# Kernel tuning notes

Measured on AMD Instinct MI355X. Metric: run time of the kernel, lower is better.

## Reference

```python
import jax, jax.numpy as jnp
import numpy as np

S, B, D, H, L = 1024, 2, 1024, 16, 4
HD = D // H            # 64
MLP = 4 * D            # 4096
EPS = 1e-5


def _ln(x, w, b):
    m = x.mean(-1, keepdims=True)
    v = ((x - m) ** 2).mean(-1, keepdims=True)
    return (x - m) * jax.lax.rsqrt(v + EPS) * w + b


def _rotate_half(x):
    h = x.shape[-1] // 2
    return jnp.concatenate([-x[..., h:], x[..., :h]], axis=-1)


def _rope(t, cos, sin):
    # t: (B, S, H, HD); cos/sin: (S, HD) broadcast to (1, S, 1, HD)
    return t * cos[None, :, None, :] + _rotate_half(t) * sin[None, :, None, :]


def setup_inputs() -> dict:
    key = jax.random.key(0)
    ks = iter(jax.random.split(key, 64))

    def p(shape, scale=0.02):
        return jax.random.normal(next(ks), shape, jnp.float32) * scale

    return {
        "x": jax.random.normal(next(ks), (S, B, D), jnp.float32),
        "rotary_pos_emb": jax.random.normal(next(ks), (S, HD // 2), jnp.float32),
        # stacked per-layer params (leading dim L) for lax.scan
        "ln1_w": jnp.ones((L, D), jnp.float32), "ln1_b": jnp.zeros((L, D), jnp.float32),
        "in_w": p((L, 3 * D, D)), "in_b": jnp.zeros((L, 3 * D), jnp.float32),
        "out_w": p((L, D, D)), "out_b": jnp.zeros((L, D), jnp.float32),
        "ln2_w": jnp.ones((L, D), jnp.float32), "ln2_b": jnp.zeros((L, D), jnp.float32),
        "fc_w": p((L, MLP, D)), "fc_b": jnp.zeros((L, MLP), jnp.float32),
        "cp_w": p((L, D, MLP)), "cp_b": jnp.zeros((L, D), jnp.float32),
        # attention pooling head (qkv_bias=False in CrossAttention)
        "pn_q_w": jnp.ones((D,), jnp.float32), "pn_q_b": jnp.zeros((D,), jnp.float32),
        "pn_k_w": jnp.ones((D,), jnp.float32), "pn_k_b": jnp.zeros((D,), jnp.float32),
        "pn_v_w": jnp.ones((D,), jnp.float32), "pn_v_b": jnp.zeros((D,), jnp.float32),
        "pq_w": p((D, D)), "pk_w": p((D, D)), "pv_w": p((D, D)),
        "pp_w": p((D, D)), "pp_b": jnp.zeros((D,), jnp.float32),
    }


def reference(x, rotary_pos_emb, ln1_w, ln1_b, in_w, in_b, out_w, out_b,
              ln2_w, ln2_b, fc_w, fc_b, cp_w, cp_b,
              pn_q_w, pn_q_b, pn_k_w, pn_k_b, pn_v_w, pn_v_b,
              pq_w, pk_w, pv_w, pp_w, pp_b):
    # freqs (S, HD/2) -> cos/sin tiled twice along last dim: (S, HD)
    cos = jnp.tile(jnp.cos(rotary_pos_emb), (1, 2))
    sin = jnp.tile(jnp.sin(rotary_pos_emb), (1, 2))
    scale = 1.0 / np.sqrt(HD).astype(np.float32)

    def layer(h, p):
        l1w, l1b, iw, ib, ow, ob, l2w, l2b, fw, fb, cw, cb = p
        a = _ln(h, l1w, l1b)
        qkv = jnp.einsum('sbd,ed->sbe', a, iw) + ib           # (S,B,3D)
        qkv = qkv.reshape(S, B, 3, H, HD)
        q = jnp.transpose(qkv[:, :, 0], (1, 0, 2, 3))          # (B,S,H,HD)
        k = jnp.transpose(qkv[:, :, 1], (1, 0, 2, 3))
        v = jnp.transpose(qkv[:, :, 2], (1, 0, 2, 3))
        q = _rope(q, cos, sin)
        k = _rope(k, cos, sin)
        q, k, v = (t.transpose(0, 2, 1, 3) for t in (q, k, v))  # (B,H,S,HD)
        attn = jax.nn.softmax(jnp.einsum('bhsd,bhtd->bhst', q, k) * scale, axis=-1)
        o = jnp.einsum('bhst,bhtd->bhsd', attn, v)
        o = o.transpose(2, 0, 1, 3).reshape(S, B, D)           # back to (S,B,D)
        h = h + jnp.einsum('sbd,ed->sbe', o, ow) + ob          # residual + out_proj
        m = _ln(h, l2w, l2b)
        m = jax.nn.gelu(jnp.einsum('sbd,ed->sbe', m, fw) + fb, approximate=False)
        h = h + jnp.einsum('sbe,de->sbd', m, cw) + cb          # residual + c_proj
        return h, None

    h, _ = jax.lax.scan(layer, x, (ln1_w, ln1_b, in_w, in_b, out_w, out_b,
                                   ln2_w, ln2_b, fc_w, fc_b, cp_w, cp_b))

    # AttentionPoolingBlock: mean-pooled single query, cross-attend over tokens
    t = h.transpose(1, 0, 2)                                   # (B,N,C)
    xq = _ln(t.mean(1, keepdims=True), pn_q_w, pn_q_b)         # (B,1,C)
    xk = _ln(t, pn_k_w, pn_k_b)
    xv = _ln(t, pn_v_w, pn_v_b)
    q = (xq @ pq_w.T).reshape(B, 1, H, HD).transpose(0, 2, 1, 3)   # (B,H,1,HD)
    k = (xk @ pk_w.T).reshape(B, S, H, HD).transpose(0, 2, 1, 3)
    v = (xv @ pv_w.T).reshape(B, S, H, HD).transpose(0, 2, 1, 3)
    a = jax.nn.softmax(jnp.einsum('bhqd,bhtd->bhqt', q, k) * scale, axis=-1)
    o = jnp.einsum('bhqt,bhtd->bhqd', a, v).transpose(0, 2, 1, 3).reshape(B, 1, D)
    return (o @ pp_w.T + pp_b)[:, 0]                           # (B, D)
```

## Files before the change

### kernel.cpp

```cpp
#include <hip/hip_runtime.h>
#include <math.h>

#define S_LEN  1024
#define BATCH  2
#define DMODEL 1024
#define NHEAD  16
#define HDIM   64
#define NLAYER 4
#define MLPD   4096
#define MROWS  (S_LEN*BATCH)

typedef __attribute__((ext_vector_type(8))) short bf16x8_t;
typedef __attribute__((ext_vector_type(4))) float f32x4_t;

__device__ __forceinline__ unsigned short f2bf(float f) {
  union { float f; unsigned u; } c; c.f = f;
  return (unsigned short)((c.u + 0x7FFFu + ((c.u >> 16) & 1u)) >> 16);
}
__device__ __forceinline__ float bf2f(unsigned short u) {
  union { unsigned u; float f; } c; c.u = ((unsigned)u) << 16; return c.f;
}

__device__ __forceinline__ void gl_lds16(const unsigned short* g, unsigned short* l) {
  __builtin_amdgcn_global_load_lds(
      (const __attribute__((address_space(1))) unsigned int*)(g),
      (__attribute__((address_space(3))) unsigned int*)(l), 16, 0, 0);
}

__global__ __launch_bounds__(256) void w2bf_kernel(const float* __restrict__ src,
    unsigned short* __restrict__ dst, int n) {
  const int i = (blockIdx.x * 256 + threadIdx.x) * 8;
  if (i >= n) return;
  float4 v0 = *(const float4*)(src + i);
  float4 v1 = *(const float4*)(src + i + 4);
  ushort4 u0, u1;
  u0.x = f2bf(v0.x); u0.y = f2bf(v0.y); u0.z = f2bf(v0.z); u0.w = f2bf(v0.w);
  u1.x = f2bf(v1.x); u1.y = f2bf(v1.y); u1.z = f2bf(v1.z); u1.w = f2bf(v1.w);
  *(ushort4*)(dst + i)     = u0;
  *(ushort4*)(dst + i + 4) = u1;
}

template<bool BF16OUT>
__global__ __launch_bounds__(256) void ln_kernel(const float* __restrict__ x,
    const float* __restrict__ w, const float* __restrict__ b,
    void* __restrict__ out, float inscale) {
  const int row = blockIdx.x;
  const int tid = threadIdx.x;
  const float* xr = x + (size_t)row * DMODEL;
  float4 v = *(const float4*)(xr + tid * 4);
  v.x *= inscale; v.y *= inscale; v.z *= inscale; v.w *= inscale;
  float s1 = v.x + v.y + v.z + v.w;
  float s2 = v.x*v.x + v.y*v.y + v.z*v.z + v.w*v.w;
  #pragma unroll
  for (int off = 32; off; off >>= 1) {
    s1 += __shfl_xor(s1, off);
    s2 += __shfl_xor(s2, off);
  }
  __shared__ float as1[4], as2[4];
  if ((tid & 63) == 0) { as1[tid >> 6] = s1; as2[tid >> 6] = s2; }
  __syncthreads();
  s1 = as1[0] + as1[1] + as1[2] + as1[3];
  s2 = as2[0] + as2[1] + as2[2] + as2[3];
  const float mean = s1 * (1.0f / DMODEL);
  const float var  = s2 * (1.0f / DMODEL) - mean * mean;
  const float r = rsqrtf(var + 1e-5f);
  float4 wv = *(const float4*)(w + tid * 4);
  float4 bv = *(const float4*)(b + tid * 4);
  float o0 = (v.x - mean) * r * wv.x + bv.x;
  float o1 = (v.y - mean) * r * wv.y + bv.y;
  float o2 = (v.z - mean) * r * wv.z + bv.z;
  float o3 = (v.w - mean) * r * wv.w + bv.w;
  if (BF16OUT) {
    ushort4 u; u.x = f2bf(o0); u.y = f2bf(o1); u.z = f2bf(o2); u.w = f2bf(o3);
    *(ushort4*)((unsigned short*)out + (size_t)row * DMODEL + tid * 4) = u;
  } else {
    float4 ov; ov.x = o0; ov.y = o1; ov.z = o2; ov.w = o3;
    *(float4*)((float*)out + (size_t)row * DMODEL + tid * 4) = ov;
  }
}

template<int NS, bool ADDDEST, bool DOLN>
__global__ __launch_bounds__(256) void reduce_ln_kernel(
    const float* __restrict__ part, const float* __restrict__ bias,
    float* __restrict__ dest, const float* __restrict__ lnw,
    const float* __restrict__ lnb, unsigned short* __restrict__ lnout) {
  const int row = blockIdx.x;
  const int tid = threadIdx.x;
  const size_t off = (size_t)row * DMODEL + tid * 4;
  float4 v;
  if (ADDDEST) v = *(const float4*)(dest + off);
  else { v.x = 0.f; v.y = 0.f; v.z = 0.f; v.w = 0.f; }
  if (bias) {
    float4 b4 = *(const float4*)(bias + tid * 4);
    v.x += b4.x; v.y += b4.y; v.z += b4.z; v.w += b4.w;
  }
  #pragma unroll
  for (int z = 0; z < NS; ++z) {
    float4 p = *(const float4*)(part + (size_t)z * (MROWS * DMODEL) + off);
    v.x += p.x; v.y += p.y; v.z += p.z; v.w += p.w;
  }
  *(float4*)(dest + off) = v;
  if (DOLN) {
    float s1 = v.x + v.y + v.z + v.w;
    float s2 = v.x*v.x + v.y*v.y + v.z*v.z + v.w*v.w;
    #pragma unroll
    for (int o = 32; o; o >>= 1) {
      s1 += __shfl_xor(s1, o);
      s2 += __shfl_xor(s2, o);
    }
    __shared__ float as1[4], as2[4];
    if ((tid & 63) == 0) { as1[tid >> 6] = s1; as2[tid >> 6] = s2; }
    __syncthreads();
    s1 = as1[0] + as1[1] + as1[2] + as1[3];
    s2 = as2[0] + as2[1] + as2[2] + as2[3];
    const float mean = s1 * (1.0f / DMODEL);
    const float var  = s2 * (1.0f / DMODEL) - mean * mean;
    const float r = rsqrtf(var + 1e-5f);
    float4 wv = *(const float4*)(lnw + tid * 4);
    float4 bv = *(const float4*)(lnb + tid * 4);
    ushort4 u;
    u.x = f2bf((v.x - mean) * r * wv.x + bv.x);
    u.y = f2bf((v.y - mean) * r * wv.y + bv.y);
    u.z = f2bf((v.z - mean) * r * wv.z + bv.z);
    u.w = f2bf((v.w - mean) * r * wv.w + bv.w);
    *(ushort4*)(lnout + (size_t)row * DMODEL + tid * 4) = u;
  }
}

template<int SPLIT, bool GELU, bool PARTIAL, bool OUTBF16>
__global__ __launch_bounds__(256, 3) void gemm_mfma(
    const unsigned short* __restrict__ A, const unsigned short* __restrict__ W,
    const float* __restrict__ bias, void* __restrict__ Cout,
    int M, int N, int K) {
  constexpr int BK = 32;
  __shared__ __align__(16) unsigned short As[2][128 * BK];
  __shared__ __align__(16) unsigned short Bs[2][128 * BK];
  const int tid  = threadIdx.x;
  const int wid  = tid >> 6;
  const int lane = tid & 63;
  const int lrow = lane & 15;
  const int lq   = lane >> 4;

  const int NB = gridDim.x, MB = gridDim.y;
  const int f = blockIdx.y * NB + blockIdx.x;
  const int xcd = f & 7;
  const int idx = f >> 3;
  const int m0 = (idx % MB) * 128;
  const int n0 = (xcd + (idx / MB) * 8) * 128;

  const int wm = (wid >> 1) * 64;
  const int wn = (wid & 1) * 64;
  const int Kc = K / SPLIT;
  const int kbase = blockIdx.z * Kc;

  f32x4_t acc[4][4];
  #pragma unroll
  for (int i = 0; i < 4; ++i)
    #pragma unroll
    for (int j = 0; j < 4; ++j) acc[i][j] = (f32x4_t){0.f, 0.f, 0.f, 0.f};

  const int c1 = tid, c2 = tid + 256;
  const unsigned short* Ag1 = A + (size_t)(m0 + (c1 >> 2)) * K + kbase + (c1 & 3) * 8;
  const unsigned short* Ag2 = A + (size_t)(m0 + (c2 >> 2)) * K + kbase + (c2 & 3) * 8;
  const unsigned short* Wg1 = W + (size_t)(n0 + (c1 >> 2)) * K + kbase + (c1 & 3) * 8;
  const unsigned short* Wg2 = W + (size_t)(n0 + (c2 >> 2)) * K + kbase + (c2 & 3) * 8;
  const int l1 = c1 * 8, l2 = c2 * 8;

  gl_lds16(Ag1, &As[0][l1]);
  gl_lds16(Ag2, &As[0][l2]);
  gl_lds16(Wg1, &Bs[0][l1]);
  gl_lds16(Wg2, &Bs[0][l2]);
  __syncthreads();

  int cur = 0;
  for (int k0 = 0; k0 < Kc; k0 += BK) {
    if (k0 + BK < Kc) {
      gl_lds16(Ag1 + k0 + BK, &As[cur ^ 1][l1]);
      gl_lds16(Ag2 + k0 + BK, &As[cur ^ 1][l2]);
      gl_lds16(Wg1 + k0 + BK, &Bs[cur ^ 1][l1]);
      gl_lds16(Wg2 + k0 + BK, &Bs[cur ^ 1][l2]);
    }

    bf16x8_t af[4], bfr[4];
    #pragma unroll
    for (int i = 0; i < 4; ++i)
      af[i] = *(const bf16x8_t*)&As[cur][(wm + i * 16 + lrow) * BK + lq * 8];
    #pragma unroll
    for (int j = 0; j < 4; ++j)
      bfr[j] = *(const bf16x8_t*)&Bs[cur][(wn + j * 16 + lrow) * BK + lq * 8];
    #pragma unroll
    for (int i = 0; i < 4; ++i)
      #pragma unroll
      for (int j = 0; j < 4; ++j)
        acc[i][j] = __builtin_amdgcn_mfma_f32_16x16x32_bf16(af[i], bfr[j], acc[i][j], 0, 0, 0);

    __syncthreads();
    cur ^= 1;
  }

  const size_t zoff = PARTIAL ? (size_t)blockIdx.z * ((size_t)M * N) : 0;
  float bj[4];
  #pragma unroll
  for (int j = 0; j < 4; ++j)
    bj[j] = (bias && (SPLIT == 1 || blockIdx.z == 0)) ? bias[n0 + wn + j * 16 + lrow] : 0.f;
  #pragma unroll
  for (int i = 0; i < 4; ++i) {
    #pragma unroll
    for (int r = 0; r < 4; ++r) {
      const int row = m0 + wm + i * 16 + lq * 4 + r;
      const size_t idx2 = (size_t)row * N + n0 + wn + lrow;
      #pragma unroll
      for (int j = 0; j < 4; ++j) {
        float val = acc[i][j][r] + bj[j];
        if (GELU)
          val = 0.5f * val * (1.0f + erff(val * 0.70710678118654752f));
        if (PARTIAL)
          ((float*)Cout)[zoff + idx2 + j * 16] = val;
        else if (OUTBF16)
          ((unsigned short*)Cout)[idx2 + j * 16] = f2bf(val);
        else
          ((float*)Cout)[idx2 + j * 16] = val;
      }
    }
  }
}

__global__ __launch_bounds__(256) void rope_kernel(const unsigned short* __restrict__ qkv,
    const float* __restrict__ rot, unsigned short* __restrict__ qt,
    unsigned short* __restrict__ kt, unsigned short* __restrict__ vt) {
  const int idx = blockIdx.x * 256 + threadIdx.x;
  const int d  = idx & 63;
  const int hh = (idx >> 6) & 15;
  const int m  = idx >> 10;
  const int s  = m >> 1;
  const int b  = m & 1;
  const float f  = rot[s * 32 + (d & 31)];
  const float cs = cosf(f);
  const float sn = sinf(f);
  const float sign = (d < 32) ? -1.0f : 1.0f;
  const size_t base  = (size_t)m * 3072 + hh * 64;
  const int bh = b * 16 + hh;
  const size_t obase = (((size_t)bh * 1024 + s) << 6) + d;
  float qv = bf2f(qkv[base + d]);
  float qp = bf2f(qkv[base + (d ^ 32)]);
  qt[obase] = f2bf(qv * cs + sign * qp * sn);
  float kv = bf2f(qkv[base + 1024 + d]);
  float kp = bf2f(qkv[base + 1024 + (d ^ 32)]);
  kt[obase] = f2bf(kv * cs + sign * kp * sn);
  vt[(((size_t)bh * 64 + d) << 10) + s] = qkv[base + 2048 + d];
}

__global__ __launch_bounds__(256, 2) void attn_kernel(
    const unsigned short* __restrict__ q, const unsigned short* __restrict__ k,
    const unsigned short* __restrict__ vtr, unsigned short* __restrict__ o) {
  const int tid  = threadIdx.x;
  const int wid  = tid >> 6;
  const int lane = tid & 63;
  const int col  = lane & 15;
  const int quad = lane >> 4;
  const int bh   = blockIdx.x >> 4;
  const int qw   = (blockIdx.x & 15) * 64 + wid * 16;

  __shared__ __align__(16) unsigned short Ks[64 * 72];
  __shared__ __align__(16) unsigned short Vs[64 * 72];
  __shared__ __align__(16) unsigned short Pl_[4][16 * 72];
  unsigned short* Pl = Pl_[wid];

  const unsigned short* kb = k   + ((size_t)bh << 16);
  const unsigned short* vb = vtr + ((size_t)bh << 16);

  bf16x8_t qa0, qa1;
  {
    const unsigned short* qp = q + ((((size_t)bh << 10) + qw + col) << 6) + quad * 8;
    qa0 = *(const bf16x8_t*)(qp);
    qa1 = *(const bf16x8_t*)(qp + 32);
  }

  f32x4_t oacc[4];
  #pragma unroll
  for (int j = 0; j < 4; ++j) oacc[j] = (f32x4_t){0.f, 0.f, 0.f, 0.f};
  float mr[4] = {-3.0e38f, -3.0e38f, -3.0e38f, -3.0e38f};
  float lr[4] = {0.f, 0.f, 0.f, 0.f};

  const int srow = tid >> 2;
  const int scol = (tid & 3) * 16;

  for (int t0 = 0; t0 < 1024; t0 += 64) {
    __syncthreads();
    {
      const unsigned short* gk = kb + (size_t)(t0 + srow) * 64 + scol;
      const unsigned short* gv = vb + (size_t)srow * 1024 + t0 + scol;
      uint4 ka = *(const uint4*)(gk);
      uint4 kc = *(const uint4*)(gk + 8);
      uint4 va = *(const uint4*)(gv);
      uint4 vc = *(const uint4*)(gv + 8);
      *(uint4*)&Ks[srow * 72 + scol]     = ka;
      *(uint4*)&Ks[srow * 72 + scol + 8] = kc;
      *(uint4*)&Vs[srow * 72 + scol]     = va;
      *(uint4*)&Vs[srow * 72 + scol + 8] = vc;
    }
    __syncthreads();

    f32x4_t sc[4];
    #pragma unroll
    for (int j = 0; j < 4; ++j) {
      bf16x8_t kf0 = *(const bf16x8_t*)&Ks[(j * 16 + col) * 72 + quad * 8];
      bf16x8_t kf1 = *(const bf16x8_t*)&Ks[(j * 16 + col) * 72 + quad * 8 + 32];
      f32x4_t c = (f32x4_t){0.f, 0.f, 0.f, 0.f};
      c = __builtin_amdgcn_mfma_f32_16x16x32_bf16(qa0, kf0, c, 0, 0, 0);
      c = __builtin_amdgcn_mfma_f32_16x16x32_bf16(qa1, kf1, c, 0, 0, 0);
      sc[j] = c;
    }

    #pragma unroll
    for (int r = 0; r < 4; ++r) {
      float s0 = sc[0][r] * 0.125f, s1 = sc[1][r] * 0.125f;
      float s2 = sc[2][r] * 0.125f, s3 = sc[3][r] * 0.125f;
      float rm = fmaxf(fmaxf(s0, s1), fmaxf(s2, s3));
      rm = fmaxf(rm, __shfl_xor(rm, 1));
      rm = fmaxf(rm, __shfl_xor(rm, 2));
      rm = fmaxf(rm, __shfl_xor(rm, 4));
      rm = fmaxf(rm, __shfl_xor(rm, 8));
      const float mn = fmaxf(mr[r], rm);
      const float alpha = __expf(mr[r] - mn);
      mr[r] = mn;
      const float p0 = __expf(s0 - mn), p1 = __expf(s1 - mn);
      const float p2 = __expf(s2 - mn), p3 = __expf(s3 - mn);
      float rs = p0 + p1 + p2 + p3;
      rs += __shfl_xor(rs, 1);
      rs += __shfl_xor(rs, 2);
      rs += __shfl_xor(rs, 4);
      rs += __shfl_xor(rs, 8);
      lr[r] = lr[r] * alpha + rs;
      #pragma unroll
      for (int j = 0; j < 4; ++j) oacc[j][r] *= alpha;
      const int prow = (quad * 4 + r) * 72;
      Pl[prow +  0 + col] = f2bf(p0);
      Pl[prow + 16 + col] = f2bf(p1);
      Pl[prow + 32 + col] = f2bf(p2);
      Pl[prow + 48 + col] = f2bf(p3);
    }

    bf16x8_t pa0 = *(const bf16x8_t*)&Pl[col * 72 + quad * 8];
    bf16x8_t pa1 = *(const bf16x8_t*)&Pl[col * 72 + quad * 8 + 32];
    #pragma unroll
    for (int j = 0; j < 4; ++j) {
      bf16x8_t vf0 = *(const bf16x8_t*)&Vs[(j * 16 + col) * 72 + quad * 8];
      bf16x8_t vf1 = *(const bf16x8_t*)&Vs[(j * 16 + col) * 72 + quad * 8 + 32];
      oacc[j] = __builtin_amdgcn_mfma_f32_16x16x32_bf16(pa0, vf0, oacc[j], 0, 0, 0);
      oacc[j] = __builtin_amdgcn_mfma_f32_16x16x32_bf16(pa1, vf1, oacc[j], 0, 0, 0);
    }
  }

  const int b = bh >> 4, hh = bh & 15;
  #pragma unroll
  for (int r = 0; r < 4; ++r) {
    const float inv = 1.0f / lr[r];
    const int sq = qw + quad * 4 + r;
    unsigned short* orow = o + (((size_t)sq * 2 + b) << 10) + hh * 64;
    #pragma unroll
    for (int j = 0; j < 4; ++j)
      orow[j * 16 + col] = f2bf(oacc[j][r] * inv);
  }
}

__global__ __launch_bounds__(256) void mean_kernel(const float* __restrict__ h,
    float* __restrict__ tsum) {
  const int idx = blockIdx.x * 256 + threadIdx.x;
  const int bd = idx & 2047;
  const int sc = idx >> 11;
  const int b = bd >> 10, d = bd & 1023;
  float sm = 0.f;
  for (int s = sc * 128; s < sc * 128 + 128; ++s)
    sm += h[(((size_t)s * 2 + b) << 10) + d];
  atomicAdd(&tsum[bd], sm);
}

__global__ __launch_bounds__(256) void smallmv_kernel(const float* __restrict__ in,
    const float* __restrict__ W, const float* __restrict__ bias,
    float* __restrict__ out) {
  const int lane = threadIdx.x & 63;
  const int n = blockIdx.x * 4 + (threadIdx.x >> 6);
  const int b = blockIdx.y;
  const float* wr = W + (size_t)n * 1024;
  const float* xr = in + (size_t)b * 1024;
  float sm = 0.f;
  #pragma unroll
  for (int j = 0; j < 4; ++j) {
    float4 wv = *(const float4*)(wr + lane * 4 + j * 256);
    float4 xv = *(const float4*)(xr + lane * 4 + j * 256);
    sm += wv.x * xv.x + wv.y * xv.y + wv.z * xv.z + wv.w * xv.w;
  }
  #pragma unroll
  for (int off = 32; off; off >>= 1) sm += __shfl_xor(sm, off);
  if (lane == 0) out[(size_t)b * 1024 + n] = sm + (bias ? bias[n] : 0.f);
}

__global__ __launch_bounds__(256) void pool_attn_part(const float* __restrict__ q,
    const float* __restrict__ k, const float* __restrict__ v,
    float* __restrict__ part) {
  const int wid  = (blockIdx.x * 256 + threadIdx.x) >> 6;
  const int lane = threadIdx.x & 63;
  const int bh = wid >> 4, kblk = wid & 15;
  const int b = bh >> 4, hh = bh & 15;
  const float qd = q[(size_t)b * 1024 + hh * 64 + lane];
  float mx = -3.0e38f, l = 0.f, acc = 0.f;
  for (int t = kblk * 64; t < kblk * 64 + 64; ++t) {
    const size_t ro = (((size_t)t * 2 + b) << 10) + hh * 64 + lane;
    float p = qd * k[ro];
    p += __shfl_xor(p, 32); p += __shfl_xor(p, 16); p += __shfl_xor(p, 8);
    p += __shfl_xor(p, 4);  p += __shfl_xor(p, 2);  p += __shfl_xor(p, 1);
    const float sc = p * 0.125f;
    const float mn = fmaxf(mx, sc);
    const float alpha = __expf(mx - mn);
    const float w = __expf(sc - mn);
    acc = acc * alpha + w * v[ro];
    l   = l * alpha + w;
    mx  = mn;
  }
  float* pp = part + (size_t)wid * 68;
  if (lane == 0) { pp[0] = mx; pp[1] = l; }
  pp[4 + lane] = acc;
}

__global__ __launch_bounds__(256) void pool_attn_comb(const float* __restrict__ part,
    float* __restrict__ o) {
  const int wid  = (blockIdx.x * 256 + threadIdx.x) >> 6;
  const int lane = threadIdx.x & 63;
  const float* pb = part + (size_t)wid * 16 * 68;
  float M = -3.0e38f;
  #pragma unroll
  for (int w = 0; w < 16; ++w) M = fmaxf(M, pb[w * 68]);
  float L = 0.f, O = 0.f;
  #pragma unroll
  for (int w = 0; w < 16; ++w) {
    const float e = __expf(pb[w * 68] - M);
    L += e * pb[w * 68 + 1];
    O += e * pb[w * 68 + 4 + lane];
  }
  const int b = wid >> 4, hh = wid & 15;
  o[(size_t)b * 1024 + hh * 64 + lane] = O / L;
}

extern "C" void kernel_launch(void* const* d_in, const int* in_sizes, int n_in,
                              void* d_out, int out_size, void* d_ws, size_t ws_size,
                              hipStream_t stream) {
  (void)in_sizes; (void)n_in; (void)out_size; (void)ws_size;
  const float* x     = (const float*)d_in[0];
  const float* rot   = (const float*)d_in[1];
  const float* ln1_w = (const float*)d_in[2];
  const float* ln1_b = (const float*)d_in[3];
  const float* in_w  = (const float*)d_in[4];
  const float* in_b  = (const float*)d_in[5];
  const float* out_w = (const float*)d_in[6];
  const float* out_b = (const float*)d_in[7];
  const float* ln2_w = (const float*)d_in[8];
  const float* ln2_b = (const float*)d_in[9];
  const float* fc_w  = (const float*)d_in[10];
  const float* fc_b  = (const float*)d_in[11];
  const float* cp_w  = (const float*)d_in[12];
  const float* cp_b  = (const float*)d_in[13];
  const float* pn_q_w = (const float*)d_in[14];
  const float* pn_q_b = (const float*)d_in[15];
  const float* pn_k_w = (const float*)d_in[16];
  const float* pn_k_b = (const float*)d_in[17];
  const float* pn_v_w = (const float*)d_in[18];
  const float* pn_v_b = (const float*)d_in[19];
  const float* pq_w  = (const float*)d_in[20];
  const float* pk_w  = (const float*)d_in[21];
  const float* pv_w  = (const float*)d_in[22];
  const float* pp_w  = (const float*)d_in[23];
  const float* pp_b  = (const float*)d_in[24];

  float* ws = (float*)d_ws;
  const size_t M1 = 1u << 20;
  float* h  = ws;
  float* a  = ws + 2 * M1;
  float* r1 = ws + 4 * M1;
  float* qt = ws + 12 * M1;
  float* kt = ws + 14 * M1;
  float* vt = ws + 16 * M1;
  float* o  = ws + 18 * M1;
  float* wbf = ws + 20 * M1;
  unsigned short* a_bf  = (unsigned short*)a;
  unsigned short* r1_bf = (unsigned short*)r1;
  unsigned short* o_bf  = (unsigned short*)o;
  unsigned short* qt_bf = (unsigned short*)qt;
  unsigned short* kt_bf = (unsigned short*)kt;
  unsigned short* vt_bf = (unsigned short*)vt;
  unsigned short* wb_qkv = (unsigned short*)wbf;
  unsigned short* wb_out = wb_qkv + 3145728;
  unsigned short* wb_fc  = wb_out + 1048576;
  unsigned short* wb_cp  = wb_fc  + 4194304;
  float* part_op = r1;
  float* part_cp = qt;
  float* part_pool = ws + 5 * M1;
  float* tsum  = qt;
  float* xq    = qt + 2048;
  float* qpool = qt + 4096;
  float* opool = qt + 6144;
  float* ppart = qt + 8192;

  hipMemcpyAsync(h, x, 2 * M1 * sizeof(float), hipMemcpyDeviceToDevice, stream);

  ln_kernel<true><<<MROWS, 256, 0, stream>>>(h, ln1_w, ln1_b, a_bf, 1.0f);

  for (int l = 0; l < NLAYER; ++l) {
    w2bf_kernel<<<3145728 / 2048, 256, 0, stream>>>(in_w + (size_t)l * 3145728, wb_qkv, 3145728);
    w2bf_kernel<<<1048576 / 2048, 256, 0, stream>>>(out_w + (size_t)l * 1048576, wb_out, 1048576);
    w2bf_kernel<<<4194304 / 2048, 256, 0, stream>>>(fc_w + (size_t)l * 4194304, wb_fc, 4194304);
    w2bf_kernel<<<4194304 / 2048, 256, 0, stream>>>(cp_w + (size_t)l * 4194304, wb_cp, 4194304);

    gemm_mfma<1, false, false, true><<<dim3(3072 / 128, MROWS / 128, 1), 256, 0, stream>>>(
        a_bf, wb_qkv, in_b + l * 3072, r1_bf, MROWS, 3072, 1024);
    rope_kernel<<<8192, 256, 0, stream>>>(r1_bf, rot, qt_bf, kt_bf, vt_bf);
    attn_kernel<<<512, 256, 0, stream>>>(qt_bf, kt_bf, vt_bf, o_bf);
    gemm_mfma<4, false, true, false><<<dim3(1024 / 128, MROWS / 128, 4), 256, 0, stream>>>(
        o_bf, wb_out, nullptr, part_op, MROWS, 1024, 1024);
    reduce_ln_kernel<4, true, true><<<MROWS, 256, 0, stream>>>(
        part_op, out_b + l * 1024, h, ln2_w + l * DMODEL, ln2_b + l * DMODEL, a_bf);
    gemm_mfma<1, true, false, true><<<dim3(4096 / 128, MROWS / 128, 1), 256, 0, stream>>>(
        a_bf, wb_fc, fc_b + l * 4096, r1_bf, MROWS, 4096, 1024);
    gemm_mfma<4, false, true, false><<<dim3(1024 / 128, MROWS / 128, 4), 256, 0, stream>>>(
        r1_bf, wb_cp, nullptr, part_cp, MROWS, 1024, 4096);
    if (l < NLAYER - 1)
      reduce_ln_kernel<4, true, true><<<MROWS, 256, 0, stream>>>(
          part_cp, cp_b + l * 1024, h,
          ln1_w + (l + 1) * DMODEL, ln1_b + (l + 1) * DMODEL, a_bf);
    else
      reduce_ln_kernel<4, true, false><<<MROWS, 256, 0, stream>>>(
          part_cp, cp_b + l * 1024, h, nullptr, nullptr, nullptr);
  }

  hipMemsetAsync(tsum, 0, 2048 * sizeof(float), stream);
  mean_kernel<<<64, 256, 0, stream>>>(h, tsum);
  ln_kernel<false><<<BATCH, 256, 0, stream>>>(tsum, pn_q_w, pn_q_b, xq, 1.0f / S_LEN);
  ln_kernel<true><<<MROWS, 256, 0, stream>>>(h, pn_k_w, pn_k_b, a_bf, 1.0f);
  ln_kernel<true><<<MROWS, 256, 0, stream>>>(h, pn_v_w, pn_v_b, r1_bf, 1.0f);
  smallmv_kernel<<<dim3(256, BATCH), 256, 0, stream>>>(xq, pq_w, nullptr, qpool);
  w2bf_kernel<<<1048576 / 2048, 256, 0, stream>>>(pk_w, wb_qkv, 1048576);
  w2bf_kernel<<<1048576 / 2048, 256, 0, stream>>>(pv_w, wb_out, 1048576);
  gemm_mfma<2, false, true, false><<<dim3(1024 / 128, MROWS / 128, 2), 256, 0, stream>>>(
      a_bf, wb_qkv, nullptr, part_pool, MROWS, 1024, 1024);
  reduce_ln_kernel<2, false, false><<<MROWS, 256, 0, stream>>>(
      part_pool, nullptr, kt, nullptr, nullptr, nullptr);
  gemm_mfma<2, false, true, false><<<dim3(1024 / 128, MROWS / 128, 2), 256, 0, stream>>>(
      r1_bf, wb_out, nullptr, part_pool, MROWS, 1024, 1024);
  reduce_ln_kernel<2, false, false><<<MROWS, 256, 0, stream>>>(
      part_pool, nullptr, vt, nullptr, nullptr, nullptr);
  pool_attn_part<<<128, 256, 0, stream>>>(qpool, kt, vt, ppart);
  pool_attn_comb<<<8, 256, 0, stream>>>(ppart, opool);
  smallmv_kernel<<<dim3(256, BATCH), 256, 0, stream>>>(opool, pp_w, pp_b, (float*)d_out);
}
```

Before: 1.102 ms.

## Prefetch K/V tiles into registers in attention and precompute RoPE trig table

The attention kernel now loads the next K/V tile from global memory into registers while it computes on the current tile, then writes them to shared memory after a barrier. This hides global load latency behind the MFMA work. Launch bounds are raised to 3 blocks per SM, which may increase register pressure or cause spills. RoPE cos/sin values are computed once into a workspace table instead of with cosf/sinf in each layer's rope kernel.

```diff
diff --git a/kernel.cpp b/kernel.cpp
--- a/kernel.cpp
+++ b/kernel.cpp
@@ -38,6 +38,13 @@
   u1.x = f2bf(v1.x); u1.y = f2bf(v1.y); u1.z = f2bf(v1.z); u1.w = f2bf(v1.w);
   *(ushort4*)(dst + i)     = u0;
   *(ushort4*)(dst + i + 4) = u1;
+}
+
+__global__ __launch_bounds__(256) void trig_kernel(const float* __restrict__ rot,
+    float2* __restrict__ tab) {
+  const int i = blockIdx.x * 256 + threadIdx.x;
+  const float f = rot[i];
+  tab[i] = make_float2(cosf(f), sinf(f));
 }
 
 template<bool BF16OUT>
@@ -226,7 +233,7 @@
 }
 
 __global__ __launch_bounds__(256) void rope_kernel(const unsigned short* __restrict__ qkv,
-    const float* __restrict__ rot, unsigned short* __restrict__ qt,
+    const float2* __restrict__ trig, unsigned short* __restrict__ qt,
     unsigned short* __restrict__ kt, unsigned short* __restrict__ vt) {
   const int idx = blockIdx.x * 256 + threadIdx.x;
   const int d  = idx & 63;
@@ -234,9 +241,9 @@
   const int m  = idx >> 10;
   const int s  = m >> 1;
   const int b  = m & 1;
-  const float f  = rot[s * 32 + (d & 31)];
-  const float cs = cosf(f);
-  const float sn = sinf(f);
+  const float2 t = trig[s * 32 + (d & 31)];
+  const float cs = t.x;
+  const float sn = t.y;
   const float sign = (d < 32) ? -1.0f : 1.0f;
   const size_t base  = (size_t)m * 3072 + hh * 64;
   const int bh = b * 16 + hh;
@@ -250,7 +257,7 @@
   vt[(((size_t)bh * 64 + d) << 10) + s] = qkv[base + 2048 + d];
 }
 
-__global__ __launch_bounds__(256, 2) void attn_kernel(
+__global__ __launch_bounds__(256, 3) void attn_kernel(
     const unsigned short* __restrict__ q, const unsigned short* __restrict__ k,
     const unsigned short* __restrict__ vtr, unsigned short* __restrict__ o) {
   const int tid  = threadIdx.x;
@@ -284,22 +291,34 @@
 
   const int srow = tid >> 2;
   const int scol = (tid & 3) * 16;
+  const unsigned short* gk0 = kb + (size_t)srow * 64 + scol;
+  const unsigned short* gv0 = vb + (size_t)srow * 1024 + scol;
+  unsigned short* lk0 = &Ks[srow * 72 + scol];
+  unsigned short* lv0 = &Vs[srow * 72 + scol];
+
+  {
+    uint4 ka = *(const uint4*)(gk0);
+    uint4 kc = *(const uint4*)(gk0 + 8);
+    uint4 va = *(const uint4*)(gv0);
+    uint4 vc = *(const uint4*)(gv0 + 8);
+    *(uint4*)(lk0)     = ka;
+    *(uint4*)(lk0 + 8) = kc;
+    *(uint4*)(lv0)     = va;
+    *(uint4*)(lv0 + 8) = vc;
+  }
+  __syncthreads();
 
   for (int t0 = 0; t0 < 1024; t0 += 64) {
-    __syncthreads();
-    {
-      const unsigned short* gk = kb + (size_t)(t0 + srow) * 64 + scol;
-      const unsigned short* gv = vb + (size_t)srow * 1024 + t0 + scol;
-      uint4 ka = *(const uint4*)(gk);
-      uint4 kc = *(const uint4*)(gk + 8);
-      uint4 va = *(const uint4*)(gv);
-      uint4 vc = *(const uint4*)(gv + 8);
-      *(uint4*)&Ks[srow * 72 + scol]     = ka;
-      *(uint4*)&Ks[srow * 72 + scol + 8] = kc;
-      *(uint4*)&Vs[srow * 72 + scol]     = va;
-      *(uint4*)&Vs[srow * 72 + scol + 8] = vc;
-    }
-    __syncthreads();
+    const bool more = (t0 + 64) < 1024;
+    uint4 nka, nkc, nva, nvc;
+    if (more) {
+      const unsigned short* gk = gk0 + (size_t)(t0 + 64) * 64;
+      const unsigned short* gv = gv0 + (t0 + 64);
+      nka = *(const uint4*)(gk);
+      nkc = *(const uint4*)(gk + 8);
+      nva = *(const uint4*)(gv);
+      nvc = *(const uint4*)(gv + 8);
+    }
 
     f32x4_t sc[4];
     #pragma unroll
@@ -350,6 +369,15 @@
       oacc[j] = __builtin_amdgcn_mfma_f32_16x16x32_bf16(pa0, vf0, oacc[j], 0, 0, 0);
       oacc[j] = __builtin_amdgcn_mfma_f32_16x16x32_bf16(pa1, vf1, oacc[j], 0, 0, 0);
     }
+
+    __syncthreads();
+    if (more) {
+      *(uint4*)(lk0)     = nka;
+      *(uint4*)(lk0 + 8) = nkc;
+      *(uint4*)(lv0)     = nva;
+      *(uint4*)(lv0 + 8) = nvc;
+    }
+    __syncthreads();
   }
 
   const int b = bh >> 4, hh = bh & 15;
@@ -481,6 +509,7 @@
   float* kt = ws + 14 * M1;
   float* vt = ws + 16 * M1;
   float* o  = ws + 18 * M1;
+  float* trig = ws + 19 * M1;
   float* wbf = ws + 20 * M1;
   unsigned short* a_bf  = (unsigned short*)a;
   unsigned short* r1_bf = (unsigned short*)r1;
@@ -503,6 +532,7 @@
 
   hipMemcpyAsync(h, x, 2 * M1 * sizeof(float), hipMemcpyDeviceToDevice, stream);
 
+  trig_kernel<<<128, 256, 0, stream>>>(rot, (float2*)trig);
   ln_kernel<true><<<MROWS, 256, 0, stream>>>(h, ln1_w, ln1_b, a_bf, 1.0f);
 
   for (int l = 0; l < NLAYER; ++l) {
@@ -513,7 +543,7 @@
 
     gemm_mfma<1, false, false, true><<<dim3(3072 / 128, MROWS / 128, 1), 256, 0, stream>>>(
         a_bf, wb_qkv, in_b + l * 3072, r1_bf, MROWS, 3072, 1024);
-    rope_kernel<<<8192, 256, 0, stream>>>(r1_bf, rot, qt_bf, kt_bf, vt_bf);
+    rope_kernel<<<8192, 256, 0, stream>>>(r1_bf, (const float2*)trig, qt_bf, kt_bf, vt_bf);
     attn_kernel<<<512, 256, 0, stream>>>(qt_bf, kt_bf, vt_bf, o_bf);
     gemm_mfma<4, false, true, false><<<dim3(1024 / 128, MROWS / 128, 4), 256, 0, stream>>>(
         o_bf, wb_out, nullptr, part_op, MROWS, 1024, 1024);
```

New measurement: 1.100 ms. About the same (-0.2%).
